# Optimization experiments

Measured on AMD Instinct MI355X. Metric: run time of the kernel, lower is better.

## Reference

```python
import jax, jax.numpy as jnp
import numpy as np

MU = 0.75
H = W = 256


def _bending_energy_one(pred):
    """pred: (2, 256, 256) probabilities. Returns scalar bending energy."""
    mask = (pred[1] > 0.5).astype(jnp.float32)  # (H, W) binary nucleus mask
    p = jnp.pad(mask, 1)
    # 8-neighbor count (3x3 ones kernel with zero center)
    nc = (p[:-2, :-2] + p[:-2, 1:-1] + p[:-2, 2:] +
          p[1:-1, :-2] + p[1:-1, 2:] +
          p[2:, :-2] + p[2:, 1:-1] + p[2:, 2:])
    contour = (mask == 1.0) & (nc < 8.0)  # (H, W) bool
    flat = contour.reshape(-1)            # (H*W,)
    N = flat.shape[0]
    # Stable argsort puts contour pixel indices first, in ascending
    # (row-major) order == torch.nonzero ordering. Fixed output shape.
    order = jnp.argsort(~flat, stable=True)  # (N,) int
    m = flat.sum()                            # number of contour points
    rows = (order // W).astype(jnp.float32)
    cols = (order % W).astype(jnp.float32)
    pts = jnp.stack([rows, cols], axis=-1)    # (N, 2)

    v1 = pts[1:-1] - pts[:-2]   # point - prev_point, centers 1..N-2
    v2 = pts[2:] - pts[1:-1]    # next_point - point
    cross = v1[:, 0] * v2[:, 1] - v1[:, 1] * v2[:, 0]
    dot = (v1 * v2).sum(-1)
    n1 = jnp.sqrt((v1 ** 2).sum(-1))
    n2 = jnp.sqrt((v2 ** 2).sum(-1))
    curv = jnp.where(cross == 0.0, 0.0,
                     2.0 * jnp.abs(cross) / (n1 * n2 + dot))
    delta = jnp.where(cross >= 0.0, 0.0, 1.0)
    be = (1.0 - delta + delta * MU) * curv ** 2 / (n1 + n2)
    # valid centers are indices 1..m-2 of the contour list -> j <= m-3
    j = jnp.arange(N - 2)
    valid = j <= (m - 3)
    return jnp.where(valid, be, 0.0).sum()


def setup_inputs() -> dict:
    key = jax.random.key(0)
    k1, k2 = jax.random.split(key)
    B = 128
    inp = jax.random.normal(k1, (B, 2, H, W), dtype=jnp.float32)
    tgt = jax.random.uniform(k2, (B, 2, H, W), dtype=jnp.float32)
    return {"input": inp, "target": tgt}


def reference(input, target):
    per_image = jax.vmap(_bending_energy_one)(target)  # (B,)
    return per_image.sum() / input.shape[0]
```

## Files before the change

kernel.cpp:

```cpp
#include <hip/hip_runtime.h>

#define NW 1024
#define BANDROWS 32
#define NBANDS 8
#define NSEG 8

__device__ __forceinline__ int next_set(const unsigned long long* cw, int pos) {
    int w = pos >> 6;
    int b = pos & 63;
    unsigned long long m = cw[w];
    m = (b == 63) ? 0ULL : (m & (~0ULL << (b + 1)));
    while (m == 0ULL) {
        ++w;
        if (w >= NW) return -1;
        m = cw[w];
    }
    return (w << 6) + __builtin_ctzll(m);
}

__global__ __launch_bounds__(1024)
void contour_build_kernel(const float* __restrict__ target,
                          unsigned long long* __restrict__ cwg) {
    __shared__ unsigned long long lb[(BANDROWS + 2) * 4];

    const int img  = blockIdx.x;
    const int band = blockIdx.y;
    const int tid  = threadIdx.x;
    const int wave = tid >> 6, lane = tid & 63;

    const float* imgp = target + (size_t)img * 131072 + 65536;
    const int r0 = band * BANDROWS - 1;

    for (int w = wave; w < (BANDROWS + 2) * 4; w += 16) {
        const int gr = r0 + (w >> 2);
        unsigned long long bal = 0ULL;
        if (gr >= 0 && gr <= 255) {
            float v = imgp[(gr << 8) + ((w & 3) << 6) + lane];
            bal = __ballot(v > 0.5f);
        }
        if (lane == 0) lb[w] = bal;
    }
    __syncthreads();

    if (tid < BANDROWS * 4) {
        const int k  = tid;
        const int lr = 1 + (k >> 2);
        const int wp = k & 3;
        auto get = [&](int rr, int ww) -> unsigned long long {
            return (ww < 0 || ww > 3) ? 0ULL : lb[(rr << 2) + ww];
        };
        unsigned long long A  = get(lr - 1, wp);
        unsigned long long C  = lb[(lr << 2) + wp];
        unsigned long long Bx = get(lr + 1, wp);
        unsigned long long Ap = get(lr - 1, wp - 1), An = get(lr - 1, wp + 1);
        unsigned long long Cp = get(lr,     wp - 1), Cn = get(lr,     wp + 1);
        unsigned long long Bp = get(lr + 1, wp - 1), Bn = get(lr + 1, wp + 1);
        unsigned long long interior =
            ((A  << 1) | (Ap >> 63)) & A  & ((A  >> 1) | (An << 63)) &
            ((C  << 1) | (Cp >> 63)) &      ((C  >> 1) | (Cn << 63)) &
            ((Bx << 1) | (Bp >> 63)) & Bx & ((Bx >> 1) | (Bn << 63));
        cwg[(size_t)img * NW + band * (BANDROWS * 4) + k] = C & ~interior;
    }
}

__global__ __launch_bounds__(1024)
void bending_energy_kernel(const unsigned long long* __restrict__ cwg,
                           float* __restrict__ out, float inv_b) {
#pragma clang fp contract(off)
    __shared__ unsigned long long cw[NW];
    __shared__ float wsum[16];

    const int img = blockIdx.x;
    const int seg = blockIdx.y;
    const int tid = threadIdx.x;
    const int wave = tid >> 6, lane = tid & 63;

    cw[tid] = cwg[(size_t)img * NW + tid];
    __syncthreads();

    float sum = 0.0f;
    const int chunk = seg * 1024 + tid;
    const int word = chunk >> 3, sh = (chunk & 7) << 3;
    const unsigned int byte = (unsigned int)((cw[word] >> sh) & 0xFFULL);
    if (byte) {
        int p0 = (chunk << 3) + __builtin_ctz(byte);
        const int lim = (chunk + 1) << 3;
        int p1 = next_set(cw, p0);
        int p2 = (p1 >= 0) ? next_set(cw, p1) : -1;
        while (p0 < lim && p2 >= 0) {
            float r0f = (float)(p0 >> 8), c0f = (float)(p0 & 255);
            float r1f = (float)(p1 >> 8), c1f = (float)(p1 & 255);
            float r2f = (float)(p2 >> 8), c2f = (float)(p2 & 255);
            float v1r = r1f - r0f, v1c = c1f - c0f;
            float v2r = r2f - r1f, v2c = c2f - c1f;
            float cross = v1r * v2c - v1c * v2r;
            if (cross != 0.0f) {
                float dot = v1r * v2r + v1c * v2c;
                float n1 = sqrtf(v1r * v1r + v1c * v1c);
                float n2 = sqrtf(v2r * v2r + v2c * v2c);
                float curv = (2.0f * fabsf(cross)) / (n1 * n2 + dot);
                float factor = (cross >= 0.0f) ? 1.0f : 0.75f;
                sum += (factor * (curv * curv)) / (n1 + n2);
            }
            p0 = p1; p1 = p2;
            p2 = next_set(cw, p2);
        }
    }

    for (int off = 32; off > 0; off >>= 1) sum += __shfl_down(sum, off);
    if (lane == 0) wsum[wave] = sum;
    __syncthreads();
    if (tid == 0) {
        float t = 0.0f;
        for (int i = 0; i < 16; ++i) t += wsum[i];
        atomicAdd(out, t * inv_b);
    }
}

extern "C" void kernel_launch(void* const* d_in, const int* in_sizes, int n_in,
                              void* d_out, int out_size, void* d_ws, size_t ws_size,
                              hipStream_t stream) {
    const float* target = (const float*)d_in[1];
    float* out = (float*)d_out;
    const int B = in_sizes[1] / (2 * 256 * 256);
    unsigned long long* cwg = (unsigned long long*)d_ws;

    hipMemsetAsync(out, 0, sizeof(float) * out_size, stream);
    contour_build_kernel<<<dim3(B, NBANDS), dim3(1024), 0, stream>>>(target, cwg);
    bending_energy_kernel<<<dim3(B, NSEG), dim3(1024), 0, stream>>>(cwg, out, 1.0f / (float)B);
}
```

Baseline: 151.0 us.

## Drop memset, register-window contour scan, and smaller blocks for energy kernel

The output is now zeroed inside the first kernel instead of with a separate memset. Each contour-build wave loads all four row segments with independent loads before balloting. The energy kernel no longer stages the full image bitmap in LDS. Each thread instead keeps a 128-bit register window of the bitmap and finds the next set bits from it, falling back to global reads. Blocks shrink to 256 threads with more of them. This trades LDS staging and a barrier for global/L2 reads when successors lie outside the window, and the output zeroing relies on the first kernel finishing before the second kernel's atomics.

```diff
diff --git a/kernel.cpp b/kernel.cpp
--- a/kernel.cpp
+++ b/kernel.cpp
@@ -1,93 +1,125 @@
 #include <hip/hip_runtime.h>
 
+typedef unsigned long long ull;
 #define NW 1024
-#define BANDROWS 32
-#define NBANDS 8
-#define NSEG 8
-
-__device__ __forceinline__ int next_set(const unsigned long long* cw, int pos) {
-    int w = pos >> 6;
-    int b = pos & 63;
-    unsigned long long m = cw[w];
-    m = (b == 63) ? 0ULL : (m & (~0ULL << (b + 1)));
-    while (m == 0ULL) {
-        ++w;
-        if (w >= NW) return -1;
-        m = cw[w];
-    }
-    return (w << 6) + __builtin_ctzll(m);
-}
+#define BIG (1 << 29)
 
 __global__ __launch_bounds__(1024)
 void contour_build_kernel(const float* __restrict__ target,
-                          unsigned long long* __restrict__ cwg) {
-    __shared__ unsigned long long lb[(BANDROWS + 2) * 4];
+                          ull* __restrict__ cwg,
+                          float* __restrict__ out) {
+    __shared__ ull lb[34 * 4];
 
     const int img  = blockIdx.x;
     const int band = blockIdx.y;
     const int tid  = threadIdx.x;
     const int wave = tid >> 6, lane = tid & 63;
 
+    if (img == 0 && band == 0 && tid == 0) out[0] = 0.0f;
+
     const float* imgp = target + (size_t)img * 131072 + 65536;
-    const int r0 = band * BANDROWS - 1;
+    const int r0 = band * 32 - 1;
 
-    for (int w = wave; w < (BANDROWS + 2) * 4; w += 16) {
-        const int gr = r0 + (w >> 2);
-        unsigned long long bal = 0ULL;
-        if (gr >= 0 && gr <= 255) {
-            float v = imgp[(gr << 8) + ((w & 3) << 6) + lane];
-            bal = __ballot(v > 0.5f);
+    for (int wr = wave; wr < 34; wr += 16) {
+        const int gr = r0 + wr;
+        const bool inb = (gr >= 0 && gr <= 255);
+        const float* rowp = imgp + ((size_t)(inb ? gr : 0) << 8);
+        float v0 = inb ? rowp[lane]        : 0.0f;
+        float v1 = inb ? rowp[64 + lane]   : 0.0f;
+        float v2 = inb ? rowp[128 + lane]  : 0.0f;
+        float v3 = inb ? rowp[192 + lane]  : 0.0f;
+        ull b0 = __ballot(v0 > 0.5f);
+        ull b1 = __ballot(v1 > 0.5f);
+        ull b2 = __ballot(v2 > 0.5f);
+        ull b3 = __ballot(v3 > 0.5f);
+        if (lane == 0) {
+            lb[wr * 4 + 0] = b0; lb[wr * 4 + 1] = b1;
+            lb[wr * 4 + 2] = b2; lb[wr * 4 + 3] = b3;
         }
-        if (lane == 0) lb[w] = bal;
     }
     __syncthreads();
 
-    if (tid < BANDROWS * 4) {
+    if (tid < 128) {
         const int k  = tid;
         const int lr = 1 + (k >> 2);
         const int wp = k & 3;
-        auto get = [&](int rr, int ww) -> unsigned long long {
+        auto get = [&](int rr, int ww) -> ull {
             return (ww < 0 || ww > 3) ? 0ULL : lb[(rr << 2) + ww];
         };
-        unsigned long long A  = get(lr - 1, wp);
-        unsigned long long C  = lb[(lr << 2) + wp];
-        unsigned long long Bx = get(lr + 1, wp);
-        unsigned long long Ap = get(lr - 1, wp - 1), An = get(lr - 1, wp + 1);
-        unsigned long long Cp = get(lr,     wp - 1), Cn = get(lr,     wp + 1);
-        unsigned long long Bp = get(lr + 1, wp - 1), Bn = get(lr + 1, wp + 1);
-        unsigned long long interior =
+        ull A  = get(lr - 1, wp);
+        ull C  = lb[(lr << 2) + wp];
+        ull Bx = get(lr + 1, wp);
+        ull Ap = get(lr - 1, wp - 1), An = get(lr - 1, wp + 1);
+        ull Cp = get(lr,     wp - 1), Cn = get(lr,     wp + 1);
+        ull Bp = get(lr + 1, wp - 1), Bn = get(lr + 1, wp + 1);
+        ull interior =
             ((A  << 1) | (Ap >> 63)) & A  & ((A  >> 1) | (An << 63)) &
             ((C  << 1) | (Cp >> 63)) &      ((C  >> 1) | (Cn << 63)) &
             ((Bx << 1) | (Bp >> 63)) & Bx & ((Bx >> 1) | (Bn << 63));
-        cwg[(size_t)img * NW + band * (BANDROWS * 4) + k] = C & ~interior;
+        cwg[(size_t)img * NW + band * 128 + k] = C & ~interior;
     }
 }
 
-__global__ __launch_bounds__(1024)
-void bending_energy_kernel(const unsigned long long* __restrict__ cwg,
+__device__ __forceinline__ int next_g(const ull* __restrict__ cw, int q) {
+    int w = q >> 6;
+    if (w >= NW) return BIG;
+    const int b = q & 63;
+    ull m = cw[w] >> b;
+    if (m) return q + __builtin_ctzll(m);
+    while (++w < NW) {
+        ull t = cw[w];
+        if (t) return (w << 6) + __builtin_ctzll(t);
+    }
+    return BIG;
+}
+
+__device__ __forceinline__ int win_next(ull lo, ull hi, int base,
+                                        const ull* __restrict__ cw, int apos) {
+    const int rel = apos - base;
+    if (rel < 127) {
+        const int s = rel + 1;
+        if (s < 64) {
+            ull m = lo >> s;
+            if (m) return apos + 1 + __builtin_ctzll(m);
+            if (hi) return base + 64 + __builtin_ctzll(hi);
+        } else {
+            ull m = hi >> (s - 64);
+            if (m) return apos + 1 + __builtin_ctzll(m);
+        }
+        return next_g(cw, base + 128);
+    }
+    return next_g(cw, apos + 1);
+}
+
+__global__ __launch_bounds__(256)
+void bending_energy_kernel(const ull* __restrict__ cwg,
                            float* __restrict__ out, float inv_b) {
 #pragma clang fp contract(off)
-    __shared__ unsigned long long cw[NW];
-    __shared__ float wsum[16];
+    __shared__ float wsum[4];
 
-    const int img = blockIdx.x;
-    const int seg = blockIdx.y;
-    const int tid = threadIdx.x;
-    const int wave = tid >> 6, lane = tid & 63;
+    const int img   = blockIdx.x;
+    const int chunk = blockIdx.y * 256 + threadIdx.x;
+    const int tid   = threadIdx.x;
+    const int wave  = tid >> 6, lane = tid & 63;
 
-    cw[tid] = cwg[(size_t)img * NW + tid];
-    __syncthreads();
+    const ull* cw = cwg + (size_t)img * NW;
+    const int k  = chunk >> 3;
+    const int sh = (chunk & 7) << 3;
+    const ull w0 = cw[k];
+    const ull w1 = (k + 1 < NW) ? cw[k + 1] : 0ULL;
+    const ull w2 = (k + 2 < NW) ? cw[k + 2] : 0ULL;
+    const ull lo = (w0 >> sh) | ((w1 << 1) << (63 - sh));
+    const ull hi = (w1 >> sh) | ((w2 << 1) << (63 - sh));
+    const int base = chunk << 3;
 
     float sum = 0.0f;
-    const int chunk = seg * 1024 + tid;
-    const int word = chunk >> 3, sh = (chunk & 7) << 3;
-    const unsigned int byte = (unsigned int)((cw[word] >> sh) & 0xFFULL);
+    const unsigned int byte = (unsigned int)(lo & 0xFFULL);
     if (byte) {
-        int p0 = (chunk << 3) + __builtin_ctz(byte);
-        const int lim = (chunk + 1) << 3;
-        int p1 = next_set(cw, p0);
-        int p2 = (p1 >= 0) ? next_set(cw, p1) : -1;
-        while (p0 < lim && p2 >= 0) {
+        const int lim = base + 8;
+        int p0 = base + __builtin_ctz(byte);
+        int p1 = win_next(lo, hi, base, cw, p0);
+        int p2 = (p1 < BIG) ? win_next(lo, hi, base, cw, p1) : BIG;
+        while (p0 < lim && p2 < BIG) {
             float r0f = (float)(p0 >> 8), c0f = (float)(p0 & 255);
             float r1f = (float)(p1 >> 8), c1f = (float)(p1 & 255);
             float r2f = (float)(p2 >> 8), c2f = (float)(p2 & 255);
@@ -103,7 +135,7 @@
                 sum += (factor * (curv * curv)) / (n1 + n2);
             }
             p0 = p1; p1 = p2;
-            p2 = next_set(cw, p2);
+            p2 = win_next(lo, hi, base, cw, p2);
         }
     }
 
@@ -111,8 +143,7 @@
     if (lane == 0) wsum[wave] = sum;
     __syncthreads();
     if (tid == 0) {
-        float t = 0.0f;
-        for (int i = 0; i < 16; ++i) t += wsum[i];
+        float t = wsum[0] + wsum[1] + wsum[2] + wsum[3];
         atomicAdd(out, t * inv_b);
     }
 }
@@ -123,9 +154,8 @@
     const float* target = (const float*)d_in[1];
     float* out = (float*)d_out;
     const int B = in_sizes[1] / (2 * 256 * 256);
-    unsigned long long* cwg = (unsigned long long*)d_ws;
+    ull* cwg = (ull*)d_ws;
 
-    hipMemsetAsync(out, 0, sizeof(float) * out_size, stream);
-    contour_build_kernel<<<dim3(B, NBANDS), dim3(1024), 0, stream>>>(target, cwg);
-    bending_energy_kernel<<<dim3(B, NSEG), dim3(1024), 0, stream>>>(cwg, out, 1.0f / (float)B);
+    contour_build_kernel<<<dim3(B, 8), dim3(1024), 0, stream>>>(target, cwg, out);
+    bending_energy_kernel<<<dim3(B, 32), dim3(256), 0, stream>>>(cwg, out, 1.0f / (float)B);
 }
```

Measured after the change: 184.8 us. +22.4%, slower.
